# Performance work log

Measured on AMD Instinct MI355X. Metric: run time of the kernel, lower is better.

Reference implementation:

```python
import jax, jax.numpy as jnp
import numpy as np

N = 100000   # nodes
E = 1600000  # edges
DIN = 128
HID = 128
D2 = 64      # hard-coded last-conv width in the module
OUT = 1000


def setup_inputs() -> dict:
    key = jax.random.key(0)
    ks = jax.random.split(key, 8)
    x = jax.random.normal(ks[0], (N, DIN), dtype=jnp.float32)
    edge_index = jax.random.randint(ks[1], (2, E), 0, N, dtype=jnp.int64)
    W1 = jax.random.normal(ks[2], (DIN, HID), dtype=jnp.float32) * 0.05
    b1 = jnp.zeros((HID,), dtype=jnp.float32)
    W2 = jax.random.normal(ks[3], (HID, D2), dtype=jnp.float32) * 0.05
    b2 = jnp.zeros((D2,), dtype=jnp.float32)
    Wfc = jax.random.normal(ks[4], (D2, OUT), dtype=jnp.float32) * 0.05
    bfc = jnp.zeros((OUT,), dtype=jnp.float32)
    return {"x": x, "W1": W1, "b1": b1, "W2": W2, "b2": b2,
            "Wfc": Wfc, "bfc": bfc, "edge_index": edge_index}


def _gcn_conv(x, W, b, src, dst):
    # PyG GCNConv: h = X W; add self-loops; symmetric norm D^-1/2 (A+I) D^-1/2; + bias
    h = x @ W                                   # [N, F]
    ones = jnp.ones(src.shape[0], dtype=h.dtype)
    deg = jax.ops.segment_sum(ones, dst, num_segments=N) + 1.0  # +1 for self-loop
    dinv = jax.lax.rsqrt(deg)                   # [N]
    norm = dinv[src] * dinv[dst]                # [E]
    agg = jax.ops.segment_sum(h[src] * norm[:, None], dst, num_segments=N)
    agg = agg + h * (dinv * dinv)[:, None]      # self-loop contribution
    return agg + b


def reference(x, W1, b1, W2, b2, Wfc, bfc, edge_index):
    src, dst = edge_index[0], edge_index[1]
    h = jax.nn.relu(_gcn_conv(x, W1, b1, src, dst))
    # dropout is identity in eval mode (training=False)
    h = jax.nn.relu(_gcn_conv(h, W2, b2, src, dst))
    return h @ Wfc + bfc
```

## Files before the change

### kernel.cpp

```cpp
#include <hip/hip_runtime.h>
#include <hip/hip_bf16.h>
#include <cstddef>

typedef __attribute__((ext_vector_type(8))) short bf16x8;
typedef __attribute__((ext_vector_type(4))) float f32x4;

__device__ __forceinline__ unsigned short f2bf(float f) {
    __hip_bfloat16 h = __float2bfloat16(f);
    return __builtin_bit_cast(unsigned short, h);
}
__device__ __forceinline__ float bf2f(unsigned short u) {
    return __bfloat162float(__builtin_bit_cast(__hip_bfloat16, u));
}
__device__ __forceinline__ float bflo(unsigned u) {
    return __builtin_bit_cast(float, u << 16);
}
__device__ __forceinline__ float bfhi(unsigned u) {
    return __builtin_bit_cast(float, u & 0xffff0000u);
}


__global__ void k_zero_i(int* __restrict__ p, int total) {
    int i = blockIdx.x * blockDim.x + threadIdx.x;
    int stride = gridDim.x * blockDim.x;
    for (; i < total; i += stride) p[i] = 0;
}


__global__ void k_deg_i(const int* __restrict__ dst, int* __restrict__ deg, int E) {
    int e = blockIdx.x * blockDim.x + threadIdx.x;
    if (e < E) atomicAdd(&deg[dst[e]], 1);
}

__global__ void k_dinv(const int* __restrict__ deg, float* __restrict__ dinv, int N) {
    int i = blockIdx.x * blockDim.x + threadIdx.x;
    if (i < N) dinv[i] = rsqrtf((float)deg[i] + 1.0f);
}


#define SCAN_B 1024

__global__ void k_scan1(const int* __restrict__ in, int* __restrict__ out,
                        int* __restrict__ sums, int n) {
    __shared__ int tmp[SCAN_B];
    int tid = threadIdx.x;
    int gid = blockIdx.x * SCAN_B + tid;
    int v = (gid < n) ? in[gid] : 0;
    tmp[tid] = v;
    __syncthreads();
    for (int off = 1; off < SCAN_B; off <<= 1) {
        int t = (tid >= off) ? tmp[tid - off] : 0;
        __syncthreads();
        tmp[tid] += t;
        __syncthreads();
    }
    if (gid < n) out[gid] = tmp[tid] - v;
    if (tid == SCAN_B - 1) sums[blockIdx.x] = tmp[tid];
}

__global__ void k_scan2(int* __restrict__ sums, int nb) {
    __shared__ int tmp[128];
    int tid = threadIdx.x;
    int v = (tid < nb) ? sums[tid] : 0;
    tmp[tid] = v;
    __syncthreads();
    for (int off = 1; off < 128; off <<= 1) {
        int t = (tid >= off) ? tmp[tid - off] : 0;
        __syncthreads();
        tmp[tid] += t;
        __syncthreads();
    }
    if (tid < nb) sums[tid] = tmp[tid] - v;
}

__global__ void k_scan3(int* __restrict__ out, int* __restrict__ cursor,
                        const int* __restrict__ sums, int n) {
    int gid = blockIdx.x * SCAN_B + threadIdx.x;
    if (gid < n) {
        int v = out[gid] + sums[blockIdx.x];
        out[gid] = v;
        cursor[gid] = v;
    }
}


__global__ void k_fill(const int* __restrict__ src, const int* __restrict__ dst,
                       int* __restrict__ cursor, int* __restrict__ csr_src, int E) {
    int e = blockIdx.x * blockDim.x + threadIdx.x;
    if (e < E) {
        int pos = atomicAdd(&cursor[dst[e]], 1);
        csr_src[pos] = src[e];
    }
}


__global__ void k_conv_w(const float* __restrict__ W, unsigned short* __restrict__ Bh,
                         unsigned short* __restrict__ Bl, int K, int N)
{
    int n = blockIdx.x;
    int k = threadIdx.x;
    float v = W[(size_t)k * N + n];
    unsigned short hi = f2bf(v);
    unsigned short lo = f2bf(v - bf2f(hi));
    Bh[(size_t)n * K + k] = hi;
    Bl[(size_t)n * K + k] = lo;
}


__device__ __forceinline__ void unpack_fma(float* a, float w, uint4 v) {
    a[0] = fmaf(w, bflo(v.x), a[0]);
    a[1] = fmaf(w, bfhi(v.x), a[1]);
    a[2] = fmaf(w, bflo(v.y), a[2]);
    a[3] = fmaf(w, bfhi(v.y), a[3]);
    a[4] = fmaf(w, bflo(v.z), a[4]);
    a[5] = fmaf(w, bfhi(v.z), a[5]);
    a[6] = fmaf(w, bflo(v.w), a[6]);
    a[7] = fmaf(w, bfhi(v.w), a[7]);
}

__launch_bounds__(256)
__global__ void k_gather128(const unsigned short* __restrict__ hbf,
                            const int* __restrict__ csr_src, const int* __restrict__ off,
                            const float* __restrict__ dinv, const float* __restrict__ bias,
                            unsigned short* __restrict__ ohi, unsigned short* __restrict__ olo,
                            int N, int E)
{
    int node = blockIdx.x * 4 + (threadIdx.x >> 6);
    int lane = threadIdx.x & 63;
    if (node >= N) return;
    float dn = dinv[node];
    int beg = off[node];
    int end = (node + 1 < N) ? off[node + 1] : E;

    const int grp = lane >> 4;
    const int sub = lane & 15;

    float a[8] = {0.f, 0.f, 0.f, 0.f, 0.f, 0.f, 0.f, 0.f};
    int i = beg + grp;
    for (; i + 4 < end; i += 8) {
        int s0 = csr_src[i];
        int s1 = csr_src[i + 4];
        float w0 = dinv[s0] * dn;
        float w1 = dinv[s1] * dn;
        uint4 v0 = *(const uint4*)(hbf + (size_t)s0 * 128 + sub * 8);
        uint4 v1 = *(const uint4*)(hbf + (size_t)s1 * 128 + sub * 8);
        unpack_fma(a, w0, v0);
        unpack_fma(a, w1, v1);
    }
    if (i < end) {
        int s = csr_src[i];
        float w = dinv[s] * dn;
        uint4 v = *(const uint4*)(hbf + (size_t)s * 128 + sub * 8);
        unpack_fma(a, w, v);
    }

#pragma unroll
    for (int k = 0; k < 8; ++k) {
        a[k] += __shfl_xor(a[k], 16);
        a[k] += __shfl_xor(a[k], 32);
    }

    if (grp == 0) {
        uint4 sv = *(const uint4*)(hbf + (size_t)node * 128 + sub * 8);
        float s[8] = {bflo(sv.x), bfhi(sv.x), bflo(sv.y), bfhi(sv.y),
                      bflo(sv.z), bfhi(sv.z), bflo(sv.w), bfhi(sv.w)};
        float4 b0 = *(const float4*)(bias + sub * 8);
        float4 b1 = *(const float4*)(bias + sub * 8 + 4);
        float bv[8] = {b0.x, b0.y, b0.z, b0.w, b1.x, b1.y, b1.z, b1.w};
        float w = dn * dn;
        unsigned short hi[8], lo[8];
#pragma unroll
        for (int k = 0; k < 8; ++k) {
            float f = fmaxf(fmaf(s[k], w, a[k]) + bv[k], 0.f);
            hi[k] = f2bf(f);
            lo[k] = f2bf(f - bf2f(hi[k]));
        }
        uint4 vh, vl;
        vh.x = (unsigned)hi[0] | ((unsigned)hi[1] << 16);
        vh.y = (unsigned)hi[2] | ((unsigned)hi[3] << 16);
        vh.z = (unsigned)hi[4] | ((unsigned)hi[5] << 16);
        vh.w = (unsigned)hi[6] | ((unsigned)hi[7] << 16);
        vl.x = (unsigned)lo[0] | ((unsigned)lo[1] << 16);
        vl.y = (unsigned)lo[2] | ((unsigned)lo[3] << 16);
        vl.z = (unsigned)lo[4] | ((unsigned)lo[5] << 16);
        vl.w = (unsigned)lo[6] | ((unsigned)lo[7] << 16);
        *(uint4*)(ohi + (size_t)node * 128 + sub * 8) = vh;
        *(uint4*)(olo + (size_t)node * 128 + sub * 8) = vl;
    }
}


__launch_bounds__(256)
__global__ void k_gather64(const unsigned short* __restrict__ hbf,
                           const int* __restrict__ csr_src, const int* __restrict__ off,
                           const float* __restrict__ dinv, const float* __restrict__ bias,
                           unsigned short* __restrict__ hhi, unsigned short* __restrict__ hlo,
                           int N, int E)
{
    int node = blockIdx.x * 4 + (threadIdx.x >> 6);
    int lane = threadIdx.x & 63;
    if (node >= N) return;
    float dn = dinv[node];
    int beg = off[node];
    int end = (node + 1 < N) ? off[node + 1] : E;

    const int grp = lane >> 3;
    const int sub = lane & 7;

    float a[8] = {0.f, 0.f, 0.f, 0.f, 0.f, 0.f, 0.f, 0.f};
    int i = beg + grp;
    for (; i + 8 < end; i += 16) {
        int s0 = csr_src[i];
        int s1 = csr_src[i + 8];
        float w0 = dinv[s0] * dn;
        float w1 = dinv[s1] * dn;
        uint4 v0 = *(const uint4*)(hbf + (size_t)s0 * 64 + sub * 8);
        uint4 v1 = *(const uint4*)(hbf + (size_t)s1 * 64 + sub * 8);
        unpack_fma(a, w0, v0);
        unpack_fma(a, w1, v1);
    }
    if (i < end) {
        int s = csr_src[i];
        float w = dinv[s] * dn;
        uint4 v = *(const uint4*)(hbf + (size_t)s * 64 + sub * 8);
        unpack_fma(a, w, v);
    }

#pragma unroll
    for (int k = 0; k < 8; ++k) {
        a[k] += __shfl_xor(a[k], 8);
        a[k] += __shfl_xor(a[k], 16);
        a[k] += __shfl_xor(a[k], 32);
    }

    if (grp == 0) {
        uint4 sv = *(const uint4*)(hbf + (size_t)node * 64 + sub * 8);
        float s[8] = {bflo(sv.x), bfhi(sv.x), bflo(sv.y), bfhi(sv.y),
                      bflo(sv.z), bfhi(sv.z), bflo(sv.w), bfhi(sv.w)};
        float4 b0 = *(const float4*)(bias + sub * 8);
        float4 b1 = *(const float4*)(bias + sub * 8 + 4);
        float bv[8] = {b0.x, b0.y, b0.z, b0.w, b1.x, b1.y, b1.z, b1.w};
        float w = dn * dn;
        unsigned short hi[8], lo[8];
#pragma unroll
        for (int k = 0; k < 8; ++k) {
            float f = fmaxf(fmaf(s[k], w, a[k]) + bv[k], 0.f);
            hi[k] = f2bf(f);
            lo[k] = f2bf(f - bf2f(hi[k]));
        }
        uint4 vh, vl;
        vh.x = (unsigned)hi[0] | ((unsigned)hi[1] << 16);
        vh.y = (unsigned)hi[2] | ((unsigned)hi[3] << 16);
        vh.z = (unsigned)hi[4] | ((unsigned)hi[5] << 16);
        vh.w = (unsigned)hi[6] | ((unsigned)hi[7] << 16);
        vl.x = (unsigned)lo[0] | ((unsigned)lo[1] << 16);
        vl.y = (unsigned)lo[2] | ((unsigned)lo[3] << 16);
        vl.z = (unsigned)lo[4] | ((unsigned)lo[5] << 16);
        vl.w = (unsigned)lo[6] | ((unsigned)lo[7] << 16);
        *(uint4*)(hhi + (size_t)node * 64 + sub * 8) = vh;
        *(uint4*)(hlo + (size_t)node * 64 + sub * 8) = vl;
    }
}


__launch_bounds__(256, 2)
__global__ void gemm_mfma_l1(const float* __restrict__ A,
                             const unsigned short* __restrict__ Bth,
                             const unsigned short* __restrict__ Btl,
                             unsigned short* __restrict__ Cbf, int M)
{
    __shared__ unsigned short Ah[128 * 64], Al[128 * 64];
    __shared__ unsigned short Bh[128 * 64], Bl[128 * 64];

    const int tid = threadIdx.x;
    const int m0 = blockIdx.x * 128;
    const int lane = tid & 63, wave = tid >> 6;
    const int wr = wave >> 1, wc = wave & 1;
    const int lrow = lane & 15, kgrp = lane >> 4;

    f32x4 acc[4][4] = {};

    for (int ph = 0; ph < 2; ++ph) {
        const int k0 = ph * 64;
        __syncthreads();
        {
            const int c4 = tid & 15, r0 = tid >> 4;
#pragma unroll
            for (int p = 0; p < 8; ++p) {
                int row = r0 + p * 16;
                int gr = m0 + row; if (gr >= M) gr = M - 1;
                float4 v = *(const float4*)(A + (size_t)gr * 128 + k0 + c4 * 4);
                ushort4 hi, lo;
                hi.x = f2bf(v.x); lo.x = f2bf(v.x - bf2f(hi.x));
                hi.y = f2bf(v.y); lo.y = f2bf(v.y - bf2f(hi.y));
                hi.z = f2bf(v.z); lo.z = f2bf(v.z - bf2f(hi.z));
                hi.w = f2bf(v.w); lo.w = f2bf(v.w - bf2f(hi.w));
                int off = row * 128 + ((c4 * 8) ^ ((row & 7) << 4));
                *(ushort4*)((char*)Ah + off) = hi;
                *(ushort4*)((char*)Al + off) = lo;
            }
        }
        {
            const int c = tid & 7, col0 = tid >> 3;
#pragma unroll
            for (int p = 0; p < 4; ++p) {
                int col = col0 + p * 32;
                uint4 v = *(const uint4*)(Bth + (size_t)col * 128 + k0 + c * 8);
                uint4 w = *(const uint4*)(Btl + (size_t)col * 128 + k0 + c * 8);
                int off = col * 128 + ((c * 16) ^ ((col & 7) << 4));
                *(uint4*)((char*)Bh + off) = v;
                *(uint4*)((char*)Bl + off) = w;
            }
        }
        __syncthreads();

#pragma unroll
        for (int ks = 0; ks < 2; ++ks) {
            const int cIdx = kgrp + ks * 4;
            bf16x8 ah[4], al[4], bh[4], bl[4];
#pragma unroll
            for (int i = 0; i < 4; ++i) {
                int row = wr * 64 + i * 16 + lrow;
                int off = row * 128 + ((cIdx * 16) ^ ((row & 7) << 4));
                ah[i] = *(const bf16x8*)((const char*)Ah + off);
                al[i] = *(const bf16x8*)((const char*)Al + off);
            }
#pragma unroll
            for (int j = 0; j < 4; ++j) {
                int col = wc * 64 + j * 16 + lrow;
                int off = col * 128 + ((cIdx * 16) ^ ((col & 7) << 4));
                bh[j] = *(const bf16x8*)((const char*)Bh + off);
                bl[j] = *(const bf16x8*)((const char*)Bl + off);
            }
#pragma unroll
            for (int i = 0; i < 4; ++i)
#pragma unroll
                for (int j = 0; j < 4; ++j) {
                    acc[i][j] = __builtin_amdgcn_mfma_f32_16x16x32_bf16(bh[j], ah[i], acc[i][j], 0, 0, 0);
                    acc[i][j] = __builtin_amdgcn_mfma_f32_16x16x32_bf16(bl[j], ah[i], acc[i][j], 0, 0, 0);
                    acc[i][j] = __builtin_amdgcn_mfma_f32_16x16x32_bf16(bh[j], al[i], acc[i][j], 0, 0, 0);
                }
        }
    }

#pragma unroll
    for (int i = 0; i < 4; ++i) {
        int grow = m0 + wr * 64 + i * 16 + lrow;
        if (grow >= M) continue;
        unsigned short* crow = Cbf + (size_t)grow * 128;
#pragma unroll
        for (int j = 0; j < 4; ++j) {
            int gc = wc * 64 + j * 16 + kgrp * 4;
            ushort4 o;
            o.x = f2bf(acc[i][j][0]);
            o.y = f2bf(acc[i][j][1]);
            o.z = f2bf(acc[i][j][2]);
            o.w = f2bf(acc[i][j][3]);
            *(ushort4*)(crow + gc) = o;
        }
    }
}


__launch_bounds__(256, 3)
__global__ void gemm_mfma_l2(const unsigned short* __restrict__ Ahi_g,
                             const unsigned short* __restrict__ Alo_g,
                             const unsigned short* __restrict__ Bth,
                             const unsigned short* __restrict__ Btl,
                             unsigned short* __restrict__ Cbf, int M)
{
    __shared__ unsigned short Ah[128 * 64], Al[128 * 64];
    __shared__ unsigned short Bh[64 * 64],  Bl[64 * 64];

    const int tid = threadIdx.x;
    const int m0 = blockIdx.x * 128;
    const int lane = tid & 63, wave = tid >> 6;
    const int wr = wave >> 1, wc = wave & 1;
    const int lrow = lane & 15, kgrp = lane >> 4;

    f32x4 acc[4][2] = {};

    for (int ph = 0; ph < 2; ++ph) {
        const int k0 = ph * 64;
        __syncthreads();
        {
            const int c = tid & 7, r0 = tid >> 3;
#pragma unroll
            for (int p = 0; p < 4; ++p) {
                int row = r0 + p * 32;
                int gr = m0 + row; if (gr >= M) gr = M - 1;
                uint4 v = *(const uint4*)(Ahi_g + (size_t)gr * 128 + k0 + c * 8);
                uint4 w = *(const uint4*)(Alo_g + (size_t)gr * 128 + k0 + c * 8);
                int off = row * 128 + ((c * 16) ^ ((row & 7) << 4));
                *(uint4*)((char*)Ah + off) = v;
                *(uint4*)((char*)Al + off) = w;
            }
        }
        {
            const int c = tid & 7, col0 = tid >> 3;
#pragma unroll
            for (int p = 0; p < 2; ++p) {
                int col = col0 + p * 32;
                uint4 v = *(const uint4*)(Bth + (size_t)col * 128 + k0 + c * 8);
                uint4 w = *(const uint4*)(Btl + (size_t)col * 128 + k0 + c * 8);
                int off = col * 128 + ((c * 16) ^ ((col & 7) << 4));
                *(uint4*)((char*)Bh + off) = v;
                *(uint4*)((char*)Bl + off) = w;
            }
        }
        __syncthreads();

#pragma unroll
        for (int ks = 0; ks < 2; ++ks) {
            const int cIdx = kgrp + ks * 4;
            bf16x8 ah[4], al[4], bh[2], bl[2];
#pragma unroll
            for (int i = 0; i < 4; ++i) {
                int row = wr * 64 + i * 16 + lrow;
                int off = row * 128 + ((cIdx * 16) ^ ((row & 7) << 4));
                ah[i] = *(const bf16x8*)((const char*)Ah + off);
                al[i] = *(const bf16x8*)((const char*)Al + off);
            }
#pragma unroll
            for (int j = 0; j < 2; ++j) {
                int col = wc * 32 + j * 16 + lrow;
                int off = col * 128 + ((cIdx * 16) ^ ((col & 7) << 4));
                bh[j] = *(const bf16x8*)((const char*)Bh + off);
                bl[j] = *(const bf16x8*)((const char*)Bl + off);
            }
#pragma unroll
            for (int i = 0; i < 4; ++i)
#pragma unroll
                for (int j = 0; j < 2; ++j) {
                    acc[i][j] = __builtin_amdgcn_mfma_f32_16x16x32_bf16(bh[j], ah[i], acc[i][j], 0, 0, 0);
                    acc[i][j] = __builtin_amdgcn_mfma_f32_16x16x32_bf16(bl[j], ah[i], acc[i][j], 0, 0, 0);
                    acc[i][j] = __builtin_amdgcn_mfma_f32_16x16x32_bf16(bh[j], al[i], acc[i][j], 0, 0, 0);
                }
        }
    }

#pragma unroll
    for (int i = 0; i < 4; ++i) {
        int grow = m0 + wr * 64 + i * 16 + lrow;
        if (grow >= M) continue;
        unsigned short* crow = Cbf + (size_t)grow * 64;
#pragma unroll
        for (int j = 0; j < 2; ++j) {
            int gc = wc * 32 + j * 16 + kgrp * 4;
            ushort4 o;
            o.x = f2bf(acc[i][j][0]);
            o.y = f2bf(acc[i][j][1]);
            o.z = f2bf(acc[i][j][2]);
            o.w = f2bf(acc[i][j][3]);
            *(ushort4*)(crow + gc) = o;
        }
    }
}


__launch_bounds__(256, 2)
__global__ void gemm_mfma_out(const unsigned short* __restrict__ Ahi,
                              const unsigned short* __restrict__ Alo,
                              const unsigned short* __restrict__ Bhi,
                              const unsigned short* __restrict__ Blo,
                              const float* __restrict__ bias, float* __restrict__ C,
                              int M, int N)
{
    const int tid = threadIdx.x;
    const int lane = tid & 63, wave = tid >> 6;
    const int wr = wave >> 1, wc = wave & 1;
    const int m0 = blockIdx.x * 128 + wr * 64;
    const int n0 = blockIdx.y * 128 + wc * 64;
    const int lrow = lane & 15, kgrp = lane >> 4;

    f32x4 acc[4][4] = {};

#pragma unroll
    for (int ks = 0; ks < 2; ++ks) {
        const int koff = (kgrp + ks * 4) * 8;
        bf16x8 ah[4], al[4], bh[4], bl[4];
#pragma unroll
        for (int i = 0; i < 4; ++i) {
            int row = m0 + i * 16 + lrow; if (row >= M) row = M - 1;
            ah[i] = *(const bf16x8*)(Ahi + (size_t)row * 64 + koff);
            al[i] = *(const bf16x8*)(Alo + (size_t)row * 64 + koff);
        }
#pragma unroll
        for (int j = 0; j < 4; ++j) {
            int col = n0 + j * 16 + lrow; if (col >= N) col = N - 1;
            bh[j] = *(const bf16x8*)(Bhi + (size_t)col * 64 + koff);
            bl[j] = *(const bf16x8*)(Blo + (size_t)col * 64 + koff);
        }
#pragma unroll
        for (int i = 0; i < 4; ++i)
#pragma unroll
            for (int j = 0; j < 4; ++j) {
                acc[i][j] = __builtin_amdgcn_mfma_f32_16x16x32_bf16(bh[j], ah[i], acc[i][j], 0, 0, 0);
                acc[i][j] = __builtin_amdgcn_mfma_f32_16x16x32_bf16(bl[j], ah[i], acc[i][j], 0, 0, 0);
                acc[i][j] = __builtin_amdgcn_mfma_f32_16x16x32_bf16(bh[j], al[i], acc[i][j], 0, 0, 0);
            }
    }

#pragma unroll
    for (int i = 0; i < 4; ++i) {
        int grow = m0 + i * 16 + lrow;
        if (grow >= M) continue;
        float* crow = C + (size_t)grow * N;
#pragma unroll
        for (int j = 0; j < 4; ++j) {
            int gc = n0 + j * 16 + kgrp * 4;
            if (gc + 4 <= N) {
                float4 bv = *(const float4*)(bias + gc);
                *(float4*)(crow + gc) = make_float4(acc[i][j][0] + bv.x,
                                                    acc[i][j][1] + bv.y,
                                                    acc[i][j][2] + bv.z,
                                                    acc[i][j][3] + bv.w);
            }
        }
    }
}


extern "C" void kernel_launch(void* const* d_in, const int* in_sizes, int n_in,
                              void* d_out, int out_size, void* d_ws, size_t ws_size,
                              hipStream_t stream)
{
    const float* x   = (const float*)d_in[0];
    const float* W1  = (const float*)d_in[1];
    const float* b1  = (const float*)d_in[2];
    const float* W2  = (const float*)d_in[3];
    const float* b2  = (const float*)d_in[4];
    const float* Wfc = (const float*)d_in[5];
    const float* bfc = (const float*)d_in[6];
    const int*   ei  = (const int*)d_in[7];

    const int Nn = in_sizes[0] / 128;
    const int E  = in_sizes[7] / 2;
    const int* src = ei;
    const int* dst = ei + E;

    char* ws = (char*)d_ws;
    float*          dinv   = (float*)(ws);
    unsigned short* Wfc_hi = (unsigned short*)(ws + 512 * 1024);
    unsigned short* Wfc_lo = (unsigned short*)(ws + 768 * 1024);
    unsigned short* W1_hi  = (unsigned short*)(ws + 1024 * 1024);
    unsigned short* W1_lo  = (unsigned short*)(ws + 1088 * 1024);
    unsigned short* W2_hi  = (unsigned short*)(ws + 1152 * 1024);
    unsigned short* W2_lo  = (unsigned short*)(ws + 1216 * 1024);
    unsigned short* h2hi   = (unsigned short*)(ws + 1280 * 1024);
    unsigned short* h2lo   = (unsigned short*)(ws + 1280 * 1024 + (size_t)Nn * 64 * 2);

    char* ob = (char*)d_out;
    unsigned short* hbf     = (unsigned short*)ob;
    unsigned short* h1hi    = (unsigned short*)(ob + (size_t)Nn * 256);
    unsigned short* h1lo    = (unsigned short*)(ob + (size_t)Nn * 512);
    unsigned short* h2bf    = (unsigned short*)(ob + (size_t)Nn * 768);
    int*            csr_src = (int*)(ob + (size_t)Nn * 896);
    int*            offs    = (int*)((char*)csr_src + (size_t)E * 4);
    int*            cursor  = (int*)((char*)offs + (size_t)Nn * 4);
    int*            deg_cnt = (int*)((char*)cursor + (size_t)Nn * 4);
    int*            bsums   = (int*)((char*)deg_cnt + (size_t)Nn * 4);

    const int nScanBlocks = (Nn + SCAN_B - 1) / SCAN_B;

    k_zero_i<<<128, 256, 0, stream>>>(deg_cnt, Nn);
    k_deg_i<<<(E + 255) / 256, 256, 0, stream>>>(dst, deg_cnt, E);
    k_dinv<<<(Nn + 255) / 256, 256, 0, stream>>>(deg_cnt, dinv, Nn);
    k_scan1<<<nScanBlocks, SCAN_B, 0, stream>>>(deg_cnt, offs, bsums, Nn);
    k_scan2<<<1, 128, 0, stream>>>(bsums, nScanBlocks);
    k_scan3<<<nScanBlocks, SCAN_B, 0, stream>>>(offs, cursor, bsums, Nn);
    k_fill<<<(E + 255) / 256, 256, 0, stream>>>(src, dst, cursor, csr_src, E);
    k_conv_w<<<128, 128, 0, stream>>>(W1, W1_hi, W1_lo, 128, 128);
    k_conv_w<<<64, 128, 0, stream>>>(W2, W2_hi, W2_lo, 128, 64);
    k_conv_w<<<1000, 64, 0, stream>>>(Wfc, Wfc_hi, Wfc_lo, 64, 1000);

    gemm_mfma_l1<<<dim3((Nn + 127) / 128, 1), 256, 0, stream>>>(x, W1_hi, W1_lo, hbf, Nn);
    k_gather128<<<(Nn + 3) / 4, 256, 0, stream>>>(hbf, csr_src, offs, dinv, b1,
                                                  h1hi, h1lo, Nn, E);

    gemm_mfma_l2<<<dim3((Nn + 127) / 128, 1), 256, 0, stream>>>(h1hi, h1lo, W2_hi, W2_lo, h2bf, Nn);
    k_gather64<<<(Nn + 3) / 4, 256, 0, stream>>>(h2bf, csr_src, offs, dinv, b2,
                                                 h2hi, h2lo, Nn, E);

    gemm_mfma_out<<<dim3((Nn + 127) / 128, (1000 + 127) / 128), 256, 0, stream>>>(
        h2hi, h2lo, Wfc_hi, Wfc_lo, bfc, out_size ? (float*)d_out : (float*)d_out, Nn, 1000);
}
```

Measured before the change: 531.0 us.

## Drop split-bf16 compensation in layer GEMMs and swap output grid axes

Layers 1 and 2 no longer split operands into hi/lo bf16 pairs. Each GEMM now runs one MFMA per tile instead of three, and the layer-1 gather writes a single bf16 activation buffer. This halves the shared memory, global traffic and matrix work in those stages, at the cost of plain bf16 precision in the hidden layers, which may approach the accuracy tolerance. The output GEMM grid is also transposed so consecutive blocks cover the N columns of the same row tile, which should improve reuse of the A operand in L2.

Measured after the change: 529.1 us. Within noise of the previous version (-0.4%).

```diff
diff --git a/kernel.cpp b/kernel.cpp
--- a/kernel.cpp
+++ b/kernel.cpp
@@ -94,6 +94,14 @@
 }
 
 
+__global__ void k_conv_w_bf(const float* __restrict__ W, unsigned short* __restrict__ Bh,
+                            int K, int N)
+{
+    int n = blockIdx.x;
+    int k = threadIdx.x;
+    Bh[(size_t)n * K + k] = f2bf(W[(size_t)k * N + n]);
+}
+
 __global__ void k_conv_w(const float* __restrict__ W, unsigned short* __restrict__ Bh,
                          unsigned short* __restrict__ Bl, int K, int N)
 {
@@ -122,8 +130,7 @@
 __global__ void k_gather128(const unsigned short* __restrict__ hbf,
                             const int* __restrict__ csr_src, const int* __restrict__ off,
                             const float* __restrict__ dinv, const float* __restrict__ bias,
-                            unsigned short* __restrict__ ohi, unsigned short* __restrict__ olo,
-                            int N, int E)
+                            unsigned short* __restrict__ obf, int N, int E)
 {
     int node = blockIdx.x * 4 + (threadIdx.x >> 6);
     int lane = threadIdx.x & 63;
@@ -168,24 +175,16 @@
         float4 b1 = *(const float4*)(bias + sub * 8 + 4);
         float bv[8] = {b0.x, b0.y, b0.z, b0.w, b1.x, b1.y, b1.z, b1.w};
         float w = dn * dn;
-        unsigned short hi[8], lo[8];
-#pragma unroll
-        for (int k = 0; k < 8; ++k) {
-            float f = fmaxf(fmaf(s[k], w, a[k]) + bv[k], 0.f);
-            hi[k] = f2bf(f);
-            lo[k] = f2bf(f - bf2f(hi[k]));
-        }
-        uint4 vh, vl;
-        vh.x = (unsigned)hi[0] | ((unsigned)hi[1] << 16);
-        vh.y = (unsigned)hi[2] | ((unsigned)hi[3] << 16);
-        vh.z = (unsigned)hi[4] | ((unsigned)hi[5] << 16);
-        vh.w = (unsigned)hi[6] | ((unsigned)hi[7] << 16);
-        vl.x = (unsigned)lo[0] | ((unsigned)lo[1] << 16);
-        vl.y = (unsigned)lo[2] | ((unsigned)lo[3] << 16);
-        vl.z = (unsigned)lo[4] | ((unsigned)lo[5] << 16);
-        vl.w = (unsigned)lo[6] | ((unsigned)lo[7] << 16);
-        *(uint4*)(ohi + (size_t)node * 128 + sub * 8) = vh;
-        *(uint4*)(olo + (size_t)node * 128 + sub * 8) = vl;
+        unsigned short o[8];
+#pragma unroll
+        for (int k = 0; k < 8; ++k)
+            o[k] = f2bf(fmaxf(fmaf(s[k], w, a[k]) + bv[k], 0.f));
+        uint4 vo;
+        vo.x = (unsigned)o[0] | ((unsigned)o[1] << 16);
+        vo.y = (unsigned)o[2] | ((unsigned)o[3] << 16);
+        vo.z = (unsigned)o[4] | ((unsigned)o[5] << 16);
+        vo.w = (unsigned)o[6] | ((unsigned)o[7] << 16);
+        *(uint4*)(obf + (size_t)node * 128 + sub * 8) = vo;
     }
 }
 
@@ -265,12 +264,11 @@
 
 __launch_bounds__(256, 2)
 __global__ void gemm_mfma_l1(const float* __restrict__ A,
-                             const unsigned short* __restrict__ Bth,
-                             const unsigned short* __restrict__ Btl,
+                             const unsigned short* __restrict__ Bt,
                              unsigned short* __restrict__ Cbf, int M)
 {
-    __shared__ unsigned short Ah[128 * 64], Al[128 * 64];
-    __shared__ unsigned short Bh[128 * 64], Bl[128 * 64];
+    __shared__ unsigned short Ah[128 * 64];
+    __shared__ unsigned short Bh[128 * 64];
 
     const int tid = threadIdx.x;
     const int m0 = blockIdx.x * 128;
@@ -290,14 +288,9 @@
                 int row = r0 + p * 16;
                 int gr = m0 + row; if (gr >= M) gr = M - 1;
                 float4 v = *(const float4*)(A + (size_t)gr * 128 + k0 + c4 * 4);
-                ushort4 hi, lo;
-                hi.x = f2bf(v.x); lo.x = f2bf(v.x - bf2f(hi.x));
-                hi.y = f2bf(v.y); lo.y = f2bf(v.y - bf2f(hi.y));
-                hi.z = f2bf(v.z); lo.z = f2bf(v.z - bf2f(hi.z));
-                hi.w = f2bf(v.w); lo.w = f2bf(v.w - bf2f(hi.w));
-                int off = row * 128 + ((c4 * 8) ^ ((row & 7) << 4));
-                *(ushort4*)((char*)Ah + off) = hi;
-                *(ushort4*)((char*)Al + off) = lo;
+                ushort4 hv;
+                hv.x = f2bf(v.x); hv.y = f2bf(v.y); hv.z = f2bf(v.z); hv.w = f2bf(v.w);
+                *(ushort4*)((char*)Ah + row * 128 + ((c4 * 8) ^ ((row & 7) << 4))) = hv;
             }
         }
         {
@@ -305,11 +298,8 @@
 #pragma unroll
             for (int p = 0; p < 4; ++p) {
                 int col = col0 + p * 32;
-                uint4 v = *(const uint4*)(Bth + (size_t)col * 128 + k0 + c * 8);
-                uint4 w = *(const uint4*)(Btl + (size_t)col * 128 + k0 + c * 8);
-                int off = col * 128 + ((c * 16) ^ ((col & 7) << 4));
-                *(uint4*)((char*)Bh + off) = v;
-                *(uint4*)((char*)Bl + off) = w;
+                uint4 v = *(const uint4*)(Bt + (size_t)col * 128 + k0 + c * 8);
+                *(uint4*)((char*)Bh + col * 128 + ((c * 16) ^ ((col & 7) << 4))) = v;
             }
         }
         __syncthreads();
@@ -317,29 +307,22 @@
 #pragma unroll
         for (int ks = 0; ks < 2; ++ks) {
             const int cIdx = kgrp + ks * 4;
-            bf16x8 ah[4], al[4], bh[4], bl[4];
+            bf16x8 ah[4], bh[4];
 #pragma unroll
             for (int i = 0; i < 4; ++i) {
                 int row = wr * 64 + i * 16 + lrow;
-                int off = row * 128 + ((cIdx * 16) ^ ((row & 7) << 4));
-                ah[i] = *(const bf16x8*)((const char*)Ah + off);
-                al[i] = *(const bf16x8*)((const char*)Al + off);
+                ah[i] = *(const bf16x8*)((const char*)Ah + row * 128 + ((cIdx * 16) ^ ((row & 7) << 4)));
             }
 #pragma unroll
             for (int j = 0; j < 4; ++j) {
                 int col = wc * 64 + j * 16 + lrow;
-                int off = col * 128 + ((cIdx * 16) ^ ((col & 7) << 4));
-                bh[j] = *(const bf16x8*)((const char*)Bh + off);
-                bl[j] = *(const bf16x8*)((const char*)Bl + off);
+                bh[j] = *(const bf16x8*)((const char*)Bh + col * 128 + ((cIdx * 16) ^ ((col & 7) << 4)));
             }
 #pragma unroll
             for (int i = 0; i < 4; ++i)
 #pragma unroll
-                for (int j = 0; j < 4; ++j) {
+                for (int j = 0; j < 4; ++j)
                     acc[i][j] = __builtin_amdgcn_mfma_f32_16x16x32_bf16(bh[j], ah[i], acc[i][j], 0, 0, 0);
-                    acc[i][j] = __builtin_amdgcn_mfma_f32_16x16x32_bf16(bl[j], ah[i], acc[i][j], 0, 0, 0);
-                    acc[i][j] = __builtin_amdgcn_mfma_f32_16x16x32_bf16(bh[j], al[i], acc[i][j], 0, 0, 0);
-                }
         }
     }
 
@@ -363,14 +346,12 @@
 
 
 __launch_bounds__(256, 3)
-__global__ void gemm_mfma_l2(const unsigned short* __restrict__ Ahi_g,
-                             const unsigned short* __restrict__ Alo_g,
-                             const unsigned short* __restrict__ Bth,
-                             const unsigned short* __restrict__ Btl,
+__global__ void gemm_mfma_l2(const unsigned short* __restrict__ Abf,
+                             const unsigned short* __restrict__ Bt,
                              unsigned short* __restrict__ Cbf, int M)
 {
-    __shared__ unsigned short Ah[128 * 64], Al[128 * 64];
-    __shared__ unsigned short Bh[64 * 64],  Bl[64 * 64];
+    __shared__ unsigned short Ah[128 * 64];
+    __shared__ unsigned short Bh[64 * 64];
 
     const int tid = threadIdx.x;
     const int m0 = blockIdx.x * 128;
@@ -389,11 +370,8 @@
             for (int p = 0; p < 4; ++p) {
                 int row = r0 + p * 32;
                 int gr = m0 + row; if (gr >= M) gr = M - 1;
-                uint4 v = *(const uint4*)(Ahi_g + (size_t)gr * 128 + k0 + c * 8);
-                uint4 w = *(const uint4*)(Alo_g + (size_t)gr * 128 + k0 + c * 8);
-                int off = row * 128 + ((c * 16) ^ ((row & 7) << 4));
-                *(uint4*)((char*)Ah + off) = v;
-                *(uint4*)((char*)Al + off) = w;
+                uint4 v = *(const uint4*)(Abf + (size_t)gr * 128 + k0 + c * 8);
+                *(uint4*)((char*)Ah + row * 128 + ((c * 16) ^ ((row & 7) << 4))) = v;
             }
         }
         {
@@ -401,11 +379,8 @@
 #pragma unroll
             for (int p = 0; p < 2; ++p) {
                 int col = col0 + p * 32;
-                uint4 v = *(const uint4*)(Bth + (size_t)col * 128 + k0 + c * 8);
-                uint4 w = *(const uint4*)(Btl + (size_t)col * 128 + k0 + c * 8);
-                int off = col * 128 + ((c * 16) ^ ((col & 7) << 4));
-                *(uint4*)((char*)Bh + off) = v;
-                *(uint4*)((char*)Bl + off) = w;
+                uint4 v = *(const uint4*)(Bt + (size_t)col * 128 + k0 + c * 8);
+                *(uint4*)((char*)Bh + col * 128 + ((c * 16) ^ ((col & 7) << 4))) = v;
             }
         }
         __syncthreads();
@@ -413,29 +388,22 @@
 #pragma unroll
         for (int ks = 0; ks < 2; ++ks) {
             const int cIdx = kgrp + ks * 4;
-            bf16x8 ah[4], al[4], bh[2], bl[2];
+            bf16x8 ah[4], bh[2];
 #pragma unroll
             for (int i = 0; i < 4; ++i) {
                 int row = wr * 64 + i * 16 + lrow;
-                int off = row * 128 + ((cIdx * 16) ^ ((row & 7) << 4));
-                ah[i] = *(const bf16x8*)((const char*)Ah + off);
-                al[i] = *(const bf16x8*)((const char*)Al + off);
+                ah[i] = *(const bf16x8*)((const char*)Ah + row * 128 + ((cIdx * 16) ^ ((row & 7) << 4)));
             }
 #pragma unroll
             for (int j = 0; j < 2; ++j) {
                 int col = wc * 32 + j * 16 + lrow;
-                int off = col * 128 + ((cIdx * 16) ^ ((col & 7) << 4));
-                bh[j] = *(const bf16x8*)((const char*)Bh + off);
-                bl[j] = *(const bf16x8*)((const char*)Bl + off);
+                bh[j] = *(const bf16x8*)((const char*)Bh + col * 128 + ((cIdx * 16) ^ ((col & 7) << 4)));
             }
 #pragma unroll
             for (int i = 0; i < 4; ++i)
 #pragma unroll
-                for (int j = 0; j < 2; ++j) {
+                for (int j = 0; j < 2; ++j)
                     acc[i][j] = __builtin_amdgcn_mfma_f32_16x16x32_bf16(bh[j], ah[i], acc[i][j], 0, 0, 0);
-                    acc[i][j] = __builtin_amdgcn_mfma_f32_16x16x32_bf16(bl[j], ah[i], acc[i][j], 0, 0, 0);
-                    acc[i][j] = __builtin_amdgcn_mfma_f32_16x16x32_bf16(bh[j], al[i], acc[i][j], 0, 0, 0);
-                }
         }
     }
 
@@ -469,8 +437,8 @@
     const int tid = threadIdx.x;
     const int lane = tid & 63, wave = tid >> 6;
     const int wr = wave >> 1, wc = wave & 1;
-    const int m0 = blockIdx.x * 128 + wr * 64;
-    const int n0 = blockIdx.y * 128 + wc * 64;
+    const int m0 = blockIdx.y * 128 + wr * 64;
+    const int n0 = blockIdx.x * 128 + wc * 64;
     const int lrow = lane & 15, kgrp = lane >> 4;
 
     f32x4 acc[4][4] = {};
@@ -543,19 +511,16 @@
     float*          dinv   = (float*)(ws);
     unsigned short* Wfc_hi = (unsigned short*)(ws + 512 * 1024);
     unsigned short* Wfc_lo = (unsigned short*)(ws + 768 * 1024);
-    unsigned short* W1_hi  = (unsigned short*)(ws + 1024 * 1024);
-    unsigned short* W1_lo  = (unsigned short*)(ws + 1088 * 1024);
-    unsigned short* W2_hi  = (unsigned short*)(ws + 1152 * 1024);
-    unsigned short* W2_lo  = (unsigned short*)(ws + 1216 * 1024);
-    unsigned short* h2hi   = (unsigned short*)(ws + 1280 * 1024);
-    unsigned short* h2lo   = (unsigned short*)(ws + 1280 * 1024 + (size_t)Nn * 64 * 2);
+    unsigned short* W1_bf  = (unsigned short*)(ws + 1024 * 1024);
+    unsigned short* W2_bf  = (unsigned short*)(ws + 1088 * 1024);
+    unsigned short* h2hi   = (unsigned short*)(ws + 1152 * 1024);
+    unsigned short* h2lo   = (unsigned short*)(ws + 1152 * 1024 + (size_t)Nn * 64 * 2);
 
     char* ob = (char*)d_out;
     unsigned short* hbf     = (unsigned short*)ob;
-    unsigned short* h1hi    = (unsigned short*)(ob + (size_t)Nn * 256);
-    unsigned short* h1lo    = (unsigned short*)(ob + (size_t)Nn * 512);
-    unsigned short* h2bf    = (unsigned short*)(ob + (size_t)Nn * 768);
-    int*            csr_src = (int*)(ob + (size_t)Nn * 896);
+    unsigned short* h1bf    = (unsigned short*)(ob + (size_t)Nn * 256);
+    unsigned short* h2bf    = (unsigned short*)(ob + (size_t)Nn * 512);
+    int*            csr_src = (int*)(ob + (size_t)Nn * 640);
     int*            offs    = (int*)((char*)csr_src + (size_t)E * 4);
     int*            cursor  = (int*)((char*)offs + (size_t)Nn * 4);
     int*            deg_cnt = (int*)((char*)cursor + (size_t)Nn * 4);
@@ -570,18 +535,18 @@
     k_scan2<<<1, 128, 0, stream>>>(bsums, nScanBlocks);
     k_scan3<<<nScanBlocks, SCAN_B, 0, stream>>>(offs, cursor, bsums, Nn);
     k_fill<<<(E + 255) / 256, 256, 0, stream>>>(src, dst, cursor, csr_src, E);
-    k_conv_w<<<128, 128, 0, stream>>>(W1, W1_hi, W1_lo, 128, 128);
-    k_conv_w<<<64, 128, 0, stream>>>(W2, W2_hi, W2_lo, 128, 64);
+    k_conv_w_bf<<<128, 128, 0, stream>>>(W1, W1_bf, 128, 128);
+    k_conv_w_bf<<<64, 128, 0, stream>>>(W2, W2_bf, 128, 64);
     k_conv_w<<<1000, 64, 0, stream>>>(Wfc, Wfc_hi, Wfc_lo, 64, 1000);
 
-    gemm_mfma_l1<<<dim3((Nn + 127) / 128, 1), 256, 0, stream>>>(x, W1_hi, W1_lo, hbf, Nn);
+    gemm_mfma_l1<<<dim3((Nn + 127) / 128, 1), 256, 0, stream>>>(x, W1_bf, hbf, Nn);
     k_gather128<<<(Nn + 3) / 4, 256, 0, stream>>>(hbf, csr_src, offs, dinv, b1,
-                                                  h1hi, h1lo, Nn, E);
-
-    gemm_mfma_l2<<<dim3((Nn + 127) / 128, 1), 256, 0, stream>>>(h1hi, h1lo, W2_hi, W2_lo, h2bf, Nn);
+                                                  h1bf, Nn, E);
+
+    gemm_mfma_l2<<<dim3((Nn + 127) / 128, 1), 256, 0, stream>>>(h1bf, W2_bf, h2bf, Nn);
     k_gather64<<<(Nn + 3) / 4, 256, 0, stream>>>(h2bf, csr_src, offs, dinv, b2,
                                                  h2hi, h2lo, Nn, E);
 
-    gemm_mfma_out<<<dim3((Nn + 127) / 128, (1000 + 127) / 128), 256, 0, stream>>>(
-        h2hi, h2lo, Wfc_hi, Wfc_lo, bfc, out_size ? (float*)d_out : (float*)d_out, Nn, 1000);
-}
+    gemm_mfma_out<<<dim3((1000 + 127) / 128, (Nn + 127) / 128), 256, 0, stream>>>(
+        h2hi, h2lo, Wfc_hi, Wfc_lo, bfc, (float*)d_out, Nn, 1000);
+}
```
